# Optimization experiments

Hardware: AMD Instinct MI355X
Metric: run time of the kernel (lower is better)

## Reference

```python
import jax, jax.numpy as jnp
import numpy as np

N, D_IN, N_CTRS, D_OUT = 65536, 64, 1024, 256


def setup_inputs() -> dict:
    key = jax.random.key(0)
    k_x, k_c, k_v = jax.random.split(key, 3)
    x = jax.random.normal(k_x, (N, D_IN), dtype=jnp.float32)
    # learned params: centers (init_ctrs 'random' draws from data scale), values (normal), scales s=ones
    ctrs = jax.random.normal(k_c, (N_CTRS, D_IN), dtype=jnp.float32)
    values = jax.random.normal(k_v, (N_CTRS, D_OUT), dtype=jnp.float32) * 1e-2
    s = jnp.ones((D_IN,), dtype=jnp.float32)
    return {"x": x, "ctrs": ctrs, "values": values, "s": s}


def reference(x, ctrs, values, s):
    # dist_sq[n,k] = sum_d (x[n,d]-ctrs[k,d])^2 * s[d]
    # expanded to avoid the (N, n_ctrs, d_in) broadcast intermediate:
    x_sq = jnp.einsum('nd,d->n', x * x, s)            # (N,)
    c_sq = jnp.einsum('kd,d->k', ctrs * ctrs, s)      # (K,)
    cross = jnp.einsum('nd,kd->nk', x * s, ctrs)      # (N, K)
    dist_sq = x_sq[:, None] + c_sq[None, :] - 2.0 * cross
    assignments = jax.nn.softmax(-dist_sq, axis=1)    # (N, K)
    return assignments @ values                        # (N, d_out)
```

## Files before the change

### kernel.cpp

```cpp
#include <hip/hip_runtime.h>

typedef _Float16 half_t;
typedef half_t f16x8 __attribute__((ext_vector_type(8)));
typedef float f32x4 __attribute__((ext_vector_type(4)));
typedef unsigned int u32x2 __attribute__((ext_vector_type(2)));

#define LOG2E 1.44269504088896340736f

#define NROWS 65536
#define DIN   64
#define NCTRS 1024
#define DOUT  256

#define CSWZ_OFF 0
#define CSWZ_BYTES (128 * 1024)
#define VSWZ_OFF (CSWZ_OFF + CSWZ_BYTES)
#define VSWZ_BYTES (512 * 1024)
#define CSQ_OFF  (VSWZ_OFF + VSWZ_BYTES)

#define CT_STRIDE 68

#define RESCALE_THR 8.0f

#define GLOAD_LDS16(g, l)                                                      \
  __builtin_amdgcn_global_load_lds(                                            \
      (const __attribute__((address_space(1))) void*)(const void*)(g),         \
      (__attribute__((address_space(3))) void*)(void*)(l), 16, 0, 0)

__global__ __launch_bounds__(256) void precompute_kernel(
    const float* __restrict__ ctrs, const float* __restrict__ values,
    const float* __restrict__ s, char* __restrict__ ws) {
  half_t* Cswz = (half_t*)(ws + CSWZ_OFF);
  half_t* Vswz = (half_t*)(ws + VSWZ_OFF);
  float* csq2 = (float*)(ws + CSQ_OFF);

  __shared__ half_t Vt[32 * 36];
  __shared__ half_t Ct[32 * CT_STRIDE];

  const int bid = blockIdx.x, tid = threadIdx.x;
  const int c = bid & 31, part = bid >> 5;
  const int w = tid >> 6, l = tid & 63, l4 = l >> 4, lm = l & 15;

  {
    int r = tid >> 3, f4 = tid & 7;
    float4 v = ((const float4*)values)[(size_t)(c * 32 + r) * 64 + part * 8 + f4];
    half_t* d = Vt + r * 36 + f4 * 4;
    d[0] = (half_t)v.x; d[1] = (half_t)v.y;
    d[2] = (half_t)v.z; d[3] = (half_t)v.w;
  }
  if (part == 0) {
#pragma unroll
    for (int i = 0; i < 2; ++i) {
      int idx = i * 256 + tid;
      int r = idx >> 4, c4 = (idx & 15) * 4;
      float4 v = ((const float4*)ctrs)[(size_t)(c * 32 + r) * 16 + (idx & 15)];
      Ct[r * CT_STRIDE + c4 + 0] = (half_t)v.x;
      Ct[r * CT_STRIDE + c4 + 1] = (half_t)v.y;
      Ct[r * CT_STRIDE + c4 + 2] = (half_t)v.z;
      Ct[r * CT_STRIDE + c4 + 3] = (half_t)v.w;
    }
    {
      int k = tid >> 3, dg = (tid & 7) * 8;
      const float* cp = ctrs + (size_t)(c * 32 + k) * DIN + dg;
      float acc = 0.0f;
#pragma unroll
      for (int j = 0; j < 8; ++j) acc = fmaf(cp[j] * cp[j], s[dg + j], acc);
      acc += __shfl_xor(acc, 1);
      acc += __shfl_xor(acc, 2);
      acc += __shfl_xor(acc, 4);
      if ((tid & 7) == 0) csq2[c * 32 + k] = acc * LOG2E;
    }
  }
  __syncthreads();

  if (w < 2) {
    int sl = part * 2 + w;
    f16x8 v;
#pragma unroll
    for (int j = 0; j < 8; ++j) v[j] = Vt[(l4 * 8 + j) * 36 + w * 16 + lm];
    *(f16x8*)(Vswz + ((c * 16 + sl) * 64 + l) * 8) = v;
  }
  if (part == 0) {
    int ct = w >> 1, kt = w & 1;
    f16x8 v;
#pragma unroll
    for (int j = 0; j < 8; ++j)
      v[j] = Ct[(ct * 16 + lm) * CT_STRIDE + kt * 32 + l4 * 8 + j];
    *(f16x8*)(Cswz + ((c * 4 + w) * 64 + l) * 8) = v;
  }
}

__global__ __launch_bounds__(256, 2) void attn_kernel(
    const float* __restrict__ x, const float* __restrict__ s,
    const char* __restrict__ ws, float* __restrict__ out) {
  const char* Craw = ws + CSWZ_OFF;
  const char* Vraw = ws + VSWZ_OFF;
  const char* csqg = ws + CSQ_OFF;

  __shared__ __attribute__((aligned(16))) char vbuf[3][16384];
  __shared__ __attribute__((aligned(16))) char cbuf[4][4096];
  __shared__ __attribute__((aligned(16))) float csq_l[1024];

  const int tid = threadIdx.x;
  const int w = tid >> 6, l = tid & 63, l4 = l >> 4, lm = l & 15;
  const int rowbase = blockIdx.x * 128 + w * 32;

#define STAGE_V(chunk, bufidx)                                                 \
  do {                                                                         \
    const char* _s = Vraw + (size_t)(chunk) * 16384;                           \
    char* _d = vbuf[bufidx];                                                   \
    _Pragma("unroll") for (int _i = 0; _i < 4; ++_i)                           \
        GLOAD_LDS16(_s + _i * 4096 + tid * 16, _d + _i * 4096 + w * 1024);     \
  } while (0)
#define STAGE_C(chunk, bufidx)                                                 \
  GLOAD_LDS16(Craw + (size_t)(chunk) * 4096 + tid * 16,                        \
              (char*)cbuf[bufidx] + w * 1024)

  STAGE_V(0, 0);
  STAGE_C(0, 0);
  STAGE_C(1, 1);
  GLOAD_LDS16(csqg + tid * 16, (char*)csq_l + w * 1024);
  __builtin_amdgcn_sched_barrier(0);

  f16x8 A[2][2];
#pragma unroll
  for (int rt = 0; rt < 2; ++rt) {
#pragma unroll
    for (int kt = 0; kt < 2; ++kt) {
      int din = kt * 32 + l4 * 8;
      const float* src = x + (size_t)(rowbase + rt * 16 + lm) * DIN + din;
      f16x8 a;
#pragma unroll
      for (int j = 0; j < 8; ++j) a[j] = (half_t)(src[j] * s[din + j]);
      A[rt][kt] = a;
    }
  }

  f16x8 ones;
#pragma unroll
  for (int j = 0; j < 8; ++j) ones[j] = (lm == 0) ? (half_t)1.0f : (half_t)0.0f;

  __syncthreads();

  f32x4 t[2][2];
  {
    const char* cb = cbuf[0];
    f16x8 b0 = *(const f16x8*)(cb + 0 * 1024 + l * 16);
    f16x8 b1 = *(const f16x8*)(cb + 1 * 1024 + l * 16);
    f16x8 b2 = *(const f16x8*)(cb + 2 * 1024 + l * 16);
    f16x8 b3 = *(const f16x8*)(cb + 3 * 1024 + l * 16);
#pragma unroll
    for (int rt = 0; rt < 2; ++rt) {
      f32x4 a0 = {0.f, 0.f, 0.f, 0.f}, a1 = {0.f, 0.f, 0.f, 0.f};
      a0 = __builtin_amdgcn_mfma_f32_16x16x32_f16(b0, A[rt][0], a0, 0, 0, 0);
      a0 = __builtin_amdgcn_mfma_f32_16x16x32_f16(b1, A[rt][1], a0, 0, 0, 0);
      a1 = __builtin_amdgcn_mfma_f32_16x16x32_f16(b2, A[rt][0], a1, 0, 0, 0);
      a1 = __builtin_amdgcn_mfma_f32_16x16x32_f16(b3, A[rt][1], a1, 0, 0, 0);
      t[rt][0] = a0;
      t[rt][1] = a1;
    }
  }
  __builtin_amdgcn_sched_barrier(0);
  STAGE_V(1, 1);
  STAGE_C(2, 2);
  __builtin_amdgcn_sched_barrier(0);

  f32x4 O[2][16];
  f32x4 Lacc[2];
  float m[2] = {-1e30f, -1e30f};
#pragma unroll
  for (int rt = 0; rt < 2; ++rt) {
    Lacc[rt] = (f32x4){0.f, 0.f, 0.f, 0.f};
#pragma unroll
    for (int u = 0; u < 16; ++u) O[rt][u] = (f32x4){0.f, 0.f, 0.f, 0.f};
  }

  int vcur = 0;
#pragma unroll 1
  for (int c = 0; c < 32; ++c) {
    asm volatile("s_waitcnt vmcnt(5)" ::: "memory");
    __builtin_amdgcn_s_barrier();
    __builtin_amdgcn_sched_barrier(0);

    {
      int vn = (c + 2 < 32) ? c + 2 : 31;
      int cn = (c + 3 < 32) ? c + 3 : 31;
      int vnb = vcur + 2;
      if (vnb >= 3) vnb -= 3;
      STAGE_V(vn, vnb);
      STAGE_C(cn, (c + 3) & 3);
    }
    __builtin_amdgcn_sched_barrier(0);

    const char* cb = cbuf[(c + 1) & 3];
    f16x8 b0 = *(const f16x8*)(cb + 0 * 1024 + l * 16);
    f16x8 b1 = *(const f16x8*)(cb + 1 * 1024 + l * 16);
    f16x8 b2 = *(const f16x8*)(cb + 2 * 1024 + l * 16);
    f16x8 b3 = *(const f16x8*)(cb + 3 * 1024 + l * 16);
    f32x4 cs0 = *(const f32x4*)&csq_l[c * 32 + l4 * 4];
    f32x4 cs1 = *(const f32x4*)&csq_l[c * 32 + 16 + l4 * 4];

    f16x8 pb[2];
#pragma unroll
    for (int rt = 0; rt < 2; ++rt) {
      float v0[4], v1[4];
#pragma unroll
      for (int j = 0; j < 4; ++j) {
        v0[j] = fmaf(t[rt][0][j], 2.0f * LOG2E, -cs0[j]);
        v1[j] = fmaf(t[rt][1][j], 2.0f * LOG2E, -cs1[j]);
      }
      float pm = fmaxf(fmaxf(fmaxf(v0[0], v0[1]), fmaxf(v0[2], v0[3])),
                       fmaxf(fmaxf(v1[0], v1[1]), fmaxf(v1[2], v1[3])));
      pm = fmaxf(pm, __shfl_xor(pm, 16));
      pm = fmaxf(pm, __shfl_xor(pm, 32));

      if (__any(pm > m[rt] + RESCALE_THR)) {
        float mn = fmaxf(m[rt], pm);
        float f = __builtin_amdgcn_exp2f(m[rt] - mn);
        m[rt] = mn;
        Lacc[rt] *= f;
#pragma unroll
        for (int u = 0; u < 16; ++u) O[rt][u] *= f;
      }

      unsigned wds[4];
#pragma unroll
      for (int h = 0; h < 2; ++h) {
        union { half_t h2[2]; unsigned u; } qa, qb;
        qa.h2[0] = (half_t)__builtin_amdgcn_exp2f(v0[2 * h] - m[rt]);
        qa.h2[1] = (half_t)__builtin_amdgcn_exp2f(v0[2 * h + 1] - m[rt]);
        qb.h2[0] = (half_t)__builtin_amdgcn_exp2f(v1[2 * h] - m[rt]);
        qb.h2[1] = (half_t)__builtin_amdgcn_exp2f(v1[2 * h + 1] - m[rt]);
        u32x2 sw1 = __builtin_amdgcn_permlane32_swap(qa.u, qb.u, false, false);
        u32x2 sw2 = __builtin_amdgcn_permlane16_swap(sw1.x, sw1.y, false, false);
        wds[h] = sw2.x;
        wds[h + 2] = sw2.y;
      }
      union { unsigned u[4]; f16x8 v; } pk;
      pk.u[0] = wds[0]; pk.u[1] = wds[1]; pk.u[2] = wds[2]; pk.u[3] = wds[3];
      pb[rt] = pk.v;
    }

#pragma unroll
    for (int rt = 0; rt < 2; ++rt) {
      f32x4 a0 = {0.f, 0.f, 0.f, 0.f}, a1 = {0.f, 0.f, 0.f, 0.f};
      a0 = __builtin_amdgcn_mfma_f32_16x16x32_f16(b0, A[rt][0], a0, 0, 0, 0);
      a0 = __builtin_amdgcn_mfma_f32_16x16x32_f16(b1, A[rt][1], a0, 0, 0, 0);
      a1 = __builtin_amdgcn_mfma_f32_16x16x32_f16(b2, A[rt][0], a1, 0, 0, 0);
      a1 = __builtin_amdgcn_mfma_f32_16x16x32_f16(b3, A[rt][1], a1, 0, 0, 0);
      t[rt][0] = a0;
      t[rt][1] = a1;
    }

    __builtin_amdgcn_s_setprio(1);
    const char* vb = &vbuf[vcur][l * 16];
#pragma unroll
    for (int u = 0; u < 16; ++u) {
      f16x8 vf = *(const f16x8*)(vb + u * 1024);
      O[0][u] = __builtin_amdgcn_mfma_f32_16x16x32_f16(vf, pb[0], O[0][u], 0, 0, 0);
      O[1][u] = __builtin_amdgcn_mfma_f32_16x16x32_f16(vf, pb[1], O[1][u], 0, 0, 0);
    }
    Lacc[0] = __builtin_amdgcn_mfma_f32_16x16x32_f16(ones, pb[0], Lacc[0], 0, 0, 0);
    Lacc[1] = __builtin_amdgcn_mfma_f32_16x16x32_f16(ones, pb[1], Lacc[1], 0, 0, 0);
    __builtin_amdgcn_s_setprio(0);

    vcur = (vcur == 2) ? 0 : vcur + 1;
  }

#pragma unroll
  for (int rt = 0; rt < 2; ++rt) {
    float lv = __shfl(Lacc[rt][0], lm);
    float inv = 1.0f / fmaxf(lv, 1e-30f);
    float* po = out + (size_t)(rowbase + rt * 16 + lm) * DOUT + l4 * 4;
#pragma unroll
    for (int u = 0; u < 16; ++u) {
      f32x4 ov = O[rt][u] * inv;
      *(f32x4*)(po + u * 16) = ov;
    }
  }
#undef STAGE_V
#undef STAGE_C
}

extern "C" void kernel_launch(void* const* d_in, const int* in_sizes, int n_in,
                              void* d_out, int out_size, void* d_ws, size_t ws_size,
                              hipStream_t stream) {
  const float* x = (const float*)d_in[0];
  const float* ctrs = (const float*)d_in[1];
  const float* values = (const float*)d_in[2];
  const float* s = (const float*)d_in[3];
  float* out = (float*)d_out;
  char* ws = (char*)d_ws;

  hipLaunchKernelGGL(precompute_kernel, dim3(256), dim3(256), 0, stream,
                     ctrs, values, s, ws);
  hipLaunchKernelGGL(attn_kernel, dim3(512), dim3(256), 0, stream,
                     x, s, ws, out);
}
```

Measured before the change: 141.1 us.

## Replace LDS staging of centers and values with direct global register loads

Removes the shared-memory multi-buffer pipeline (global_load_lds staging plus barriers) for the centers, values and c_sq tables. Each wave now reads these straight from global memory (mostly L2-resident) into registers, prefetching the next chunk's centers one iteration ahead and loading values within the iteration. This drops the per-iteration block barrier, and the score MFMA is no longer software-pipelined one chunk ahead. The cost is four waves fetching the same values data redundantly through cache, more exposed global-load latency, and more VGPR pressure.

```diff
diff --git a/kernel.cpp b/kernel.cpp
--- a/kernel.cpp
+++ b/kernel.cpp
@@ -21,11 +21,6 @@
 #define CT_STRIDE 68
 
 #define RESCALE_THR 8.0f
-
-#define GLOAD_LDS16(g, l)                                                      \
-  __builtin_amdgcn_global_load_lds(                                            \
-      (const __attribute__((address_space(1))) void*)(const void*)(g),         \
-      (__attribute__((address_space(3))) void*)(void*)(l), 16, 0, 0)
 
 __global__ __launch_bounds__(256) void precompute_kernel(
     const float* __restrict__ ctrs, const float* __restrict__ values,
@@ -93,34 +88,13 @@
 __global__ __launch_bounds__(256, 2) void attn_kernel(
     const float* __restrict__ x, const float* __restrict__ s,
     const char* __restrict__ ws, float* __restrict__ out) {
-  const char* Craw = ws + CSWZ_OFF;
-  const char* Vraw = ws + VSWZ_OFF;
-  const char* csqg = ws + CSQ_OFF;
-
-  __shared__ __attribute__((aligned(16))) char vbuf[3][16384];
-  __shared__ __attribute__((aligned(16))) char cbuf[4][4096];
-  __shared__ __attribute__((aligned(16))) float csq_l[1024];
+  const f16x8* __restrict__ cbase = (const f16x8*)(ws + CSWZ_OFF);
+  const f16x8* __restrict__ vbase = (const f16x8*)(ws + VSWZ_OFF);
+  const float* __restrict__ csq2 = (const float*)(ws + CSQ_OFF);
 
   const int tid = threadIdx.x;
   const int w = tid >> 6, l = tid & 63, l4 = l >> 4, lm = l & 15;
   const int rowbase = blockIdx.x * 128 + w * 32;
-
-#define STAGE_V(chunk, bufidx)                                                 \
-  do {                                                                         \
-    const char* _s = Vraw + (size_t)(chunk) * 16384;                           \
-    char* _d = vbuf[bufidx];                                                   \
-    _Pragma("unroll") for (int _i = 0; _i < 4; ++_i)                           \
-        GLOAD_LDS16(_s + _i * 4096 + tid * 16, _d + _i * 4096 + w * 1024);     \
-  } while (0)
-#define STAGE_C(chunk, bufidx)                                                 \
-  GLOAD_LDS16(Craw + (size_t)(chunk) * 4096 + tid * 16,                        \
-              (char*)cbuf[bufidx] + w * 1024)
-
-  STAGE_V(0, 0);
-  STAGE_C(0, 0);
-  STAGE_C(1, 1);
-  GLOAD_LDS16(csqg + tid * 16, (char*)csq_l + w * 1024);
-  __builtin_amdgcn_sched_barrier(0);
 
   f16x8 A[2][2];
 #pragma unroll
@@ -140,15 +114,34 @@
 #pragma unroll
   for (int j = 0; j < 8; ++j) ones[j] = (lm == 0) ? (half_t)1.0f : (half_t)0.0f;
 
-  __syncthreads();
-
-  f32x4 t[2][2];
-  {
-    const char* cb = cbuf[0];
-    f16x8 b0 = *(const f16x8*)(cb + 0 * 1024 + l * 16);
-    f16x8 b1 = *(const f16x8*)(cb + 1 * 1024 + l * 16);
-    f16x8 b2 = *(const f16x8*)(cb + 2 * 1024 + l * 16);
-    f16x8 b3 = *(const f16x8*)(cb + 3 * 1024 + l * 16);
+  f32x4 O[2][16];
+  f32x4 Lacc[2];
+  float m[2] = {-1e30f, -1e30f};
+#pragma unroll
+  for (int rt = 0; rt < 2; ++rt) {
+    Lacc[rt] = (f32x4){0.f, 0.f, 0.f, 0.f};
+#pragma unroll
+    for (int u = 0; u < 16; ++u) O[rt][u] = (f32x4){0.f, 0.f, 0.f, 0.f};
+  }
+
+  f16x8 nb0 = cbase[0 * 64 + l], nb1 = cbase[1 * 64 + l];
+  f16x8 nb2 = cbase[2 * 64 + l], nb3 = cbase[3 * 64 + l];
+  f32x4 ncs0 = *(const f32x4*)(csq2 + l4 * 4);
+  f32x4 ncs1 = *(const f32x4*)(csq2 + 16 + l4 * 4);
+
+#pragma unroll 1
+  for (int c = 0; c < 32; ++c) {
+    f16x8 b0 = nb0, b1 = nb1, b2 = nb2, b3 = nb3;
+    f32x4 cs0 = ncs0, cs1 = ncs1;
+    int cn = (c < 31) ? c + 1 : 31;
+    nb0 = cbase[(cn * 4 + 0) * 64 + l];
+    nb1 = cbase[(cn * 4 + 1) * 64 + l];
+    nb2 = cbase[(cn * 4 + 2) * 64 + l];
+    nb3 = cbase[(cn * 4 + 3) * 64 + l];
+    ncs0 = *(const f32x4*)(csq2 + cn * 32 + l4 * 4);
+    ncs1 = *(const f32x4*)(csq2 + cn * 32 + 16 + l4 * 4);
+
+    f32x4 t0[2], t1[2];
 #pragma unroll
     for (int rt = 0; rt < 2; ++rt) {
       f32x4 a0 = {0.f, 0.f, 0.f, 0.f}, a1 = {0.f, 0.f, 0.f, 0.f};
@@ -156,49 +149,13 @@
       a0 = __builtin_amdgcn_mfma_f32_16x16x32_f16(b1, A[rt][1], a0, 0, 0, 0);
       a1 = __builtin_amdgcn_mfma_f32_16x16x32_f16(b2, A[rt][0], a1, 0, 0, 0);
       a1 = __builtin_amdgcn_mfma_f32_16x16x32_f16(b3, A[rt][1], a1, 0, 0, 0);
-      t[rt][0] = a0;
-      t[rt][1] = a1;
-    }
-  }
-  __builtin_amdgcn_sched_barrier(0);
-  STAGE_V(1, 1);
-  STAGE_C(2, 2);
-  __builtin_amdgcn_sched_barrier(0);
-
-  f32x4 O[2][16];
-  f32x4 Lacc[2];
-  float m[2] = {-1e30f, -1e30f};
-#pragma unroll
-  for (int rt = 0; rt < 2; ++rt) {
-    Lacc[rt] = (f32x4){0.f, 0.f, 0.f, 0.f};
-#pragma unroll
-    for (int u = 0; u < 16; ++u) O[rt][u] = (f32x4){0.f, 0.f, 0.f, 0.f};
-  }
-
-  int vcur = 0;
-#pragma unroll 1
-  for (int c = 0; c < 32; ++c) {
-    asm volatile("s_waitcnt vmcnt(5)" ::: "memory");
-    __builtin_amdgcn_s_barrier();
-    __builtin_amdgcn_sched_barrier(0);
-
-    {
-      int vn = (c + 2 < 32) ? c + 2 : 31;
-      int cn = (c + 3 < 32) ? c + 3 : 31;
-      int vnb = vcur + 2;
-      if (vnb >= 3) vnb -= 3;
-      STAGE_V(vn, vnb);
-      STAGE_C(cn, (c + 3) & 3);
-    }
-    __builtin_amdgcn_sched_barrier(0);
-
-    const char* cb = cbuf[(c + 1) & 3];
-    f16x8 b0 = *(const f16x8*)(cb + 0 * 1024 + l * 16);
-    f16x8 b1 = *(const f16x8*)(cb + 1 * 1024 + l * 16);
-    f16x8 b2 = *(const f16x8*)(cb + 2 * 1024 + l * 16);
-    f16x8 b3 = *(const f16x8*)(cb + 3 * 1024 + l * 16);
-    f32x4 cs0 = *(const f32x4*)&csq_l[c * 32 + l4 * 4];
-    f32x4 cs1 = *(const f32x4*)&csq_l[c * 32 + 16 + l4 * 4];
+      t0[rt] = a0;
+      t1[rt] = a1;
+    }
+
+    f16x8 vf[8];
+#pragma unroll
+    for (int u = 0; u < 8; ++u) vf[u] = vbase[(c * 16 + u) * 64 + l];
 
     f16x8 pb[2];
 #pragma unroll
@@ -206,8 +163,8 @@
       float v0[4], v1[4];
 #pragma unroll
       for (int j = 0; j < 4; ++j) {
-        v0[j] = fmaf(t[rt][0][j], 2.0f * LOG2E, -cs0[j]);
-        v1[j] = fmaf(t[rt][1][j], 2.0f * LOG2E, -cs1[j]);
+        v0[j] = fmaf(t0[rt][j], 2.0f * LOG2E, -cs0[j]);
+        v1[j] = fmaf(t1[rt][j], 2.0f * LOG2E, -cs1[j]);
       }
       float pm = fmaxf(fmaxf(fmaxf(v0[0], v0[1]), fmaxf(v0[2], v0[3])),
                        fmaxf(fmaxf(v1[0], v1[1]), fmaxf(v1[2], v1[3])));
@@ -241,30 +198,21 @@
       pb[rt] = pk.v;
     }
 
-#pragma unroll
-    for (int rt = 0; rt < 2; ++rt) {
-      f32x4 a0 = {0.f, 0.f, 0.f, 0.f}, a1 = {0.f, 0.f, 0.f, 0.f};
-      a0 = __builtin_amdgcn_mfma_f32_16x16x32_f16(b0, A[rt][0], a0, 0, 0, 0);
-      a0 = __builtin_amdgcn_mfma_f32_16x16x32_f16(b1, A[rt][1], a0, 0, 0, 0);
-      a1 = __builtin_amdgcn_mfma_f32_16x16x32_f16(b2, A[rt][0], a1, 0, 0, 0);
-      a1 = __builtin_amdgcn_mfma_f32_16x16x32_f16(b3, A[rt][1], a1, 0, 0, 0);
-      t[rt][0] = a0;
-      t[rt][1] = a1;
-    }
-
     __builtin_amdgcn_s_setprio(1);
-    const char* vb = &vbuf[vcur][l * 16];
-#pragma unroll
-    for (int u = 0; u < 16; ++u) {
-      f16x8 vf = *(const f16x8*)(vb + u * 1024);
-      O[0][u] = __builtin_amdgcn_mfma_f32_16x16x32_f16(vf, pb[0], O[0][u], 0, 0, 0);
-      O[1][u] = __builtin_amdgcn_mfma_f32_16x16x32_f16(vf, pb[1], O[1][u], 0, 0, 0);
+#pragma unroll
+    for (int u = 0; u < 8; ++u) {
+      O[0][u] = __builtin_amdgcn_mfma_f32_16x16x32_f16(vf[u], pb[0], O[0][u], 0, 0, 0);
+      O[1][u] = __builtin_amdgcn_mfma_f32_16x16x32_f16(vf[u], pb[1], O[1][u], 0, 0, 0);
+    }
+#pragma unroll
+    for (int u = 8; u < 16; ++u) {
+      f16x8 vfl = vbase[(c * 16 + u) * 64 + l];
+      O[0][u] = __builtin_amdgcn_mfma_f32_16x16x32_f16(vfl, pb[0], O[0][u], 0, 0, 0);
+      O[1][u] = __builtin_amdgcn_mfma_f32_16x16x32_f16(vfl, pb[1], O[1][u], 0, 0, 0);
     }
     Lacc[0] = __builtin_amdgcn_mfma_f32_16x16x32_f16(ones, pb[0], Lacc[0], 0, 0, 0);
     Lacc[1] = __builtin_amdgcn_mfma_f32_16x16x32_f16(ones, pb[1], Lacc[1], 0, 0, 0);
     __builtin_amdgcn_s_setprio(0);
-
-    vcur = (vcur == 2) ? 0 : vcur + 1;
   }
 
 #pragma unroll
@@ -278,8 +226,6 @@
       *(f32x4*)(po + u * 16) = ov;
     }
   }
-#undef STAGE_V
-#undef STAGE_C
 }
 
 extern "C" void kernel_launch(void* const* d_in, const int* in_sizes, int n_in,
```

After: 156.6 us. +11.0%, slower.
